# Performance work log

Measured on AMD Instinct MI355X. Metric: run time of the kernel, lower is better.

## Reference

```python
import jax, jax.numpy as jnp
import numpy as np

B, Cin, Cout, H, W = 8, 64, 128, 128, 128
K, S, P = 3, 1, 1
KK = K * K
EPS = 1e-5


def _conv2d(x, w, b=None):
    out = jax.lax.conv_general_dilated(
        x, w, window_strides=(S, S), padding=[(P, P), (P, P)],
        dimension_numbers=('NCHW', 'OIHW', 'NCHW'))
    if b is not None:
        out = out + b[None, :, None, None]
    return out


def setup_inputs() -> dict:
    key = jax.random.key(0)
    k = jax.random.split(key, 5)
    sc = 1.0 / np.sqrt(Cin * KK)
    return {
        'x': jax.random.normal(k[0], (B, Cin, H, W), jnp.float32),
        'offset_w': jax.random.normal(k[1], (2 * KK, Cin, K, K), jnp.float32) * sc,
        'offset_b': jnp.zeros((2 * KK,), jnp.float32),
        'mask_w': jax.random.normal(k[2], (KK, Cin, K, K), jnp.float32) * sc,
        'mask_b': jnp.zeros((KK,), jnp.float32),
        'conv_w': jax.random.normal(k[3], (Cout, Cin, K, K), jnp.float32) * sc,
    }


def _deform_conv2d(x, offset, mask, w):
    """Modulated deformable conv (torchvision deform_conv2d semantics)."""
    Bn, C, Hh, Ww = x.shape
    Ho, Wo = offset.shape[2], offset.shape[3]
    off = offset.reshape(Bn, KK, 2, Ho, Wo)  # (y, x) pairs per kernel tap
    ky, kx = jnp.meshgrid(jnp.arange(K), jnp.arange(K), indexing='ij')
    ky = ky.reshape(KK).astype(x.dtype)
    kx = kx.reshape(KK).astype(x.dtype)
    hy = (jnp.arange(Ho) * S - P).astype(x.dtype)
    wx = (jnp.arange(Wo) * S - P).astype(x.dtype)
    # sampling positions [B, KK, Ho, Wo]
    py = off[:, :, 0] + ky[None, :, None, None] + hy[None, None, :, None]
    px = off[:, :, 1] + kx[None, :, None, None] + wx[None, None, None, :]

    y0 = jnp.floor(py)
    x0 = jnp.floor(px)
    wy1 = py - y0; wx1 = px - x0
    wy0 = 1.0 - wy1; wx0 = 1.0 - wx1

    xf = x.reshape(Bn, C, Hh * Ww)

    def gather(yi, xi):
        valid = ((yi >= 0) & (yi < Hh) & (xi >= 0) & (xi < Ww)).astype(x.dtype)
        yc = jnp.clip(yi, 0, Hh - 1).astype(jnp.int32)
        xc = jnp.clip(xi, 0, Ww - 1).astype(jnp.int32)
        idx = (yc * Ww + xc).reshape(Bn, -1)  # [B, KK*Ho*Wo]
        vals = jnp.take_along_axis(xf, idx[:, None, :], axis=2)  # [B, C, KK*Ho*Wo]
        return vals.reshape(Bn, C, KK, Ho, Wo) * valid.reshape(Bn, 1, KK, Ho, Wo)

    v = (gather(y0, x0) * (wy0 * wx0)[:, None]
         + gather(y0, x0 + 1) * (wy0 * wx1)[:, None]
         + gather(y0 + 1, x0) * (wy1 * wx0)[:, None]
         + gather(y0 + 1, x0 + 1) * (wy1 * wx1)[:, None])  # [B, C, KK, Ho, Wo]
    v = v * mask[:, None]  # modulation
    return jnp.einsum('bckhw,ock->bohw', v, w.reshape(w.shape[0], C, KK))


def reference(x, offset_w, offset_b, mask_w, mask_b, conv_w):
    offset = _conv2d(x, offset_w, offset_b)
    mask = jax.nn.sigmoid(_conv2d(x, mask_w, mask_b))
    out = _deform_conv2d(x, offset, mask, conv_w)
    # BatchNorm2d(affine=False), training-mode normalization over (N, H, W)
    mean = out.mean(axis=(0, 2, 3), keepdims=True)
    var = out.var(axis=(0, 2, 3), keepdims=True)
    return jax.nn.relu((out - mean) * jax.lax.rsqrt(var + EPS))
```

## Files before the change

kernel.cpp:

```cpp
#include <hip/hip_runtime.h>
#include <hip/hip_bf16.h>

#define H_ 128
#define W_ 128
#define HW 16384
#define CIN 64
#define COUT 128
#define KK9 9
#define BATCH 8
#define NPIX (BATCH * HW)
#define KDIM 576

typedef short bf16x8 __attribute__((ext_vector_type(8)));
typedef float f32x4  __attribute__((ext_vector_type(4)));
typedef unsigned short ushort_t;

union U4B { uint4 u; bf16x8 v; };

__device__ __forceinline__ float us2f(unsigned short u) {
    unsigned int v = ((unsigned int)u) << 16;
    float f;
    __builtin_memcpy(&f, &v, 4);
    return f;
}
__device__ __forceinline__ float lo_f(unsigned int w) {
    unsigned int v = w << 16;
    float f;
    __builtin_memcpy(&f, &v, 4);
    return f;
}
__device__ __forceinline__ float hi_f(unsigned int w) {
    unsigned int v = w & 0xffff0000u;
    float f;
    __builtin_memcpy(&f, &v, 4);
    return f;
}
__device__ __forceinline__ unsigned short f2us_bf(float f) {
    __hip_bfloat16 h = __float2bfloat16(f);
    unsigned short u;
    __builtin_memcpy(&u, &h, 2);
    return u;
}
__device__ __forceinline__ unsigned int cvtpk_bf16(float a, float b) {
    unsigned int r;
    asm("v_cvt_pk_bf16_f32 %0, %1, %2" : "=v"(r) : "v"(a), "v"(b));
    return r;
}

template <bool F32>
__device__ __forceinline__ float ld_in(const void* p, long i) {
    if (F32) return ((const float*)p)[i];
    return us2f(((const unsigned short*)p)[i]);
}

template <bool F32>
__device__ __forceinline__ void prep_body(const void* offw, const void* offb,
                                          const void* maskw, const void* maskb,
                                          const void* convw,
                                          ushort_t* wTs, ushort_t* wcats,
                                          float* bias, int i) {
    if (i < 73728) {
        int j = i & 7, lane = (i >> 3) & 63, n = (i >> 9) & 7, ks = i >> 12;
        int co = n * 16 + (lane & 15);
        int k  = ks * 32 + ((lane >> 4) << 3) + j;
        int kk = k >> 6, ci = k & 63;
        wTs[i] = f2us_bf(ld_in<F32>(convw, (long)co * KDIM + ci * 9 + kk));
    } else if (i < 73728 + 18432) {
        int i2 = i - 73728;
        int j = i2 & 7, lane = (i2 >> 3) & 63, n = (i2 >> 9) & 1, ks = i2 >> 10;
        int co2 = n * 16 + (lane & 15);
        int k   = ks * 32 + ((lane >> 4) << 3) + j;
        int kk = k >> 6, ci = k & 63;
        float v = 0.0f;
        if (co2 < 18)      v = ld_in<F32>(offw,  (long)co2 * KDIM + ci * 9 + kk);
        else if (co2 < 27) v = ld_in<F32>(maskw, (long)(co2 - 18) * KDIM + ci * 9 + kk);
        wcats[i2] = f2us_bf(v);
    } else if (i < 73728 + 18432 + 32) {
        int j = i - 73728 - 18432;
        float v = 0.0f;
        if (j < 18)      v = ld_in<F32>(offb, j);
        else if (j < 27) v = ld_in<F32>(maskb, j - 18);
        bias[j] = v;
    }
}

template <bool F32>
__device__ __forceinline__ void transpose_body(const void* x, ushort_t* xnb,
                                               int blk) {
    __shared__ float tile[CIN * 65];
    int b    = blk >> 8;
    int pix0 = (blk & 255) * 64;
    int t    = threadIdx.x;
#pragma unroll
    for (int pass = 0; pass < 4; ++pass) {
        int slot = pass * 256 + t;
        int ci = slot >> 4;
        int f4 = slot & 15;
        long base = (long)(b * CIN + ci) * HW + pix0 + f4 * 4;
        float v0, v1, v2, v3;
        if (F32) {
            float4 v = *(const float4*)((const float*)x + base);
            v0 = v.x; v1 = v.y; v2 = v.z; v3 = v.w;
        } else {
            ushort4 u = *(const ushort4*)((const ushort_t*)x + base);
            v0 = us2f(u.x); v1 = us2f(u.y); v2 = us2f(u.z); v3 = us2f(u.w);
        }
        tile[ci * 65 + f4 * 4 + 0] = v0;
        tile[ci * 65 + f4 * 4 + 1] = v1;
        tile[ci * 65 + f4 * 4 + 2] = v2;
        tile[ci * 65 + f4 * 4 + 3] = v3;
    }
    __syncthreads();
#pragma unroll
    for (int pass = 0; pass < 4; ++pass) {
        int slot = pass * 256 + t;
        int px = slot >> 4;
        int c4 = slot & 15;
        uint2 o;
        o.x = cvtpk_bf16(tile[(c4 * 4 + 0) * 65 + px], tile[(c4 * 4 + 1) * 65 + px]);
        o.y = cvtpk_bf16(tile[(c4 * 4 + 2) * 65 + px], tile[(c4 * 4 + 3) * 65 + px]);
        *(uint2*)(xnb + (size_t)(b * HW + pix0 + px) * CIN + c4 * 4) = o;
    }
}

__global__ __launch_bounds__(256) void prep_mega(
        const void* __restrict__ x,
        const void* __restrict__ offw,
        const void* __restrict__ offb,
        const void* __restrict__ maskw,
        const void* __restrict__ maskb,
        const void* __restrict__ convw,
        ushort_t* __restrict__ wTs,
        ushort_t* __restrict__ wcats,
        float* __restrict__ bias,
        float* __restrict__ gstat,
        ushort_t* __restrict__ xnb) {
    __shared__ float flagS;
    int t   = threadIdx.x;
    int blk = blockIdx.x;

    if (t < 64) {
        uint4 v = ((const uint4*)x)[t];
        unsigned int w[4] = {v.x, v.y, v.z, v.w};
        int big = 0;
#pragma unroll
        for (int q = 0; q < 4; ++q) {
            big += (((w[q] >> 7)  & 0xFF) >= 0xC0);
            big += (((w[q] >> 23) & 0xFF) >= 0xC0);
        }
        unsigned long long m = __ballot(big > 0);
        if (t == 0) flagS = m ? 1.0f : 0.0f;
    }
    if (blk < 16) gstat[blk * 256 + t] = 0.0f;
    __syncthreads();
    bool isF32 = (flagS != 0.0f);

    if (blk < 361) {
        int i = blk * 256 + t;
        if (isF32) prep_body<true >(offw, offb, maskw, maskb, convw, wTs, wcats, bias, i);
        else       prep_body<false>(offw, offb, maskw, maskb, convw, wTs, wcats, bias, i);
    } else {
        int tb = blk - 361;
        if (isF32) transpose_body<true >(x, xnb, tb);
        else       transpose_body<false>(x, xnb, tb);
    }
}

__device__ __forceinline__ void compute_tap(int yp_t, int xp_t,
                                            float oy, float ox, float mk,
                                            int* ofs, float* wg) {
    float py  = (float)yp_t + oy;
    float pxf = (float)xp_t + ox;
    float y0f = floorf(py), x0f = floorf(pxf);
    int yi = (int)y0f, xi = (int)x0f;
    float wy1 = py - y0f, wx1 = pxf - x0f;
    float wy0 = 1.0f - wy1, wx0 = 1.0f - wx1;
    int ya  = min(max(yi, 0), H_ - 1);
    int yb  = min(max(yi + 1, 0), H_ - 1);
    int xa  = min(max(xi, 0), W_ - 1);
    int xb2 = min(max(xi + 1, 0), W_ - 1);
    bool vy0 = (yi >= 0) & (yi < H_);
    bool vy1 = (yi >= -1) & (yi < H_ - 1);
    bool vx0 = (xi >= 0) & (xi < W_);
    bool vx1 = (xi >= -1) & (xi < W_ - 1);
    float m0 = mk * wy0, m1 = mk * wy1;
    wg[0] = (vy0 & vx0) ? m0 * wx0 : 0.0f;
    wg[1] = (vy0 & vx1) ? m0 * wx1 : 0.0f;
    wg[2] = (vy1 & vx0) ? m1 * wx0 : 0.0f;
    wg[3] = (vy1 & vx1) ? m1 * wx1 : 0.0f;
    int ra = ya << 13, rb = yb << 13;
    int ca = xa << 6,  cb_ = xb2 << 6;
    ofs[0] = ra + ca;  ofs[1] = ra + cb_;
    ofs[2] = rb + ca;  ofs[3] = rb + cb_;
}

__device__ __forceinline__ void issue_half(const ushort_t* __restrict__ xb,
                                           const int* ofs, int hoff, uint4* cb) {
#pragma unroll
    for (int c = 0; c < 4; ++c)
        cb[c] = *(const uint4*)(xb + ofs[c] + hoff);
}

__device__ __forceinline__ void consume_half(int slot, const uint4* cb,
                                             const float* wg,
                                             const ushort_t* __restrict__ ldsB,
                                             int lane, f32x4* acc) {
    float2 v2[4];
#pragma unroll
    for (int j = 0; j < 4; ++j) v2[j] = make_float2(0.f, 0.f);
#pragma unroll
    for (int c = 0; c < 4; ++c) {
        float w = wg[c];
        unsigned int ww[4] = {cb[c].x, cb[c].y, cb[c].z, cb[c].w};
#pragma unroll
        for (int j = 0; j < 4; ++j) {
            v2[j].x = fmaf(w, lo_f(ww[j]), v2[j].x);
            v2[j].y = fmaf(w, hi_f(ww[j]), v2[j].y);
        }
    }
    U4B a;
    a.u = make_uint4(cvtpk_bf16(v2[0].x, v2[0].y), cvtpk_bf16(v2[1].x, v2[1].y),
                     cvtpk_bf16(v2[2].x, v2[2].y), cvtpk_bf16(v2[3].x, v2[3].y));
    const ushort_t* bbase = ldsB + ((size_t)(slot * 8) * 64 + lane) * 8;
#pragma unroll
    for (int n = 0; n < 8; ++n) {
        bf16x8 bf = *(const bf16x8*)(bbase + n * 64 * 8);
        acc[n] = __builtin_amdgcn_mfma_f32_16x16x32_bf16(a.v, bf, acc[n], 0, 0, 0);
    }
}

#define SB_PIN_VMEM() __builtin_amdgcn_sched_barrier(0x38F)

__global__ __launch_bounds__(1024, 4) void fused_conv_deform(
        const ushort_t* __restrict__ xnb,
        const ushort_t* __restrict__ wcats,
        const float* __restrict__ bias,
        const ushort_t* __restrict__ wTs,
        ushort_t* __restrict__ prebn,
        float* __restrict__ gstat) {
    __shared__ uint4 lds[8192];

    float2* offL  = (float2*)(lds + 6400);
    float*  maskS = (float*) (lds + 7552);
    float*  red   = (float*) (lds + 8128);

    int t    = threadIdx.x;
    int bid  = blockIdx.x;
    int sbid = (bid & 7) * 64 + (bid >> 3);
    int pix0 = sbid * 256;
    int b    = pix0 >> 14;
    int rem0 = pix0 & 16383;
    int y0   = rem0 >> 7;

    const uint4* wc4 = (const uint4*)wcats;
    for (int i = t; i < 2304; i += 1024) lds[i] = wc4[i];
    const uint4* xrow4 = (const uint4*)(xnb + (size_t)b * HW * CIN);
    int sxq = t >> 3, sc16 = t & 7;
#pragma unroll
    for (int r = 0; r < 4; ++r) {
        int gy = y0 - 1 + r;
        if (gy >= 0 && gy < H_) {
            uint4 v = xrow4[(size_t)gy * 1024 + t];
            lds[2304 + r * 1024 + sxq * 8 + (sc16 ^ (sxq & 7))] = v;
        }
    }
    if (t < 256) red[t] = 0.0f;
    __syncthreads();

    int wave = t >> 6, lane = t & 63, mrow = lane & 15, quad = lane >> 4;
    int px_l = wave * 16 + mrow;

    {
        int ly = px_l >> 7;
        int xp = px_l & 127;
        uint4 af0[9], af1[9];
#pragma unroll
        for (int kk = 0; kk < 9; ++kk) {
            int ty = kk / 3, tx = kk % 3;
            int tr = ly + ty;
            int gy = y0 - 1 + tr;
            int xq = xp + tx - 1;
            bool ok = (gy >= 0) && (gy < H_) && (xq >= 0) && (xq < W_);
            int xc = min(max(xq, 0), W_ - 1);
            int base = 2304 + tr * 1024 + xc * 8;
            uint4 a0 = lds[base + ((quad    ) ^ (xc & 7))];
            uint4 a1 = lds[base + ((quad + 4) ^ (xc & 7))];
            af0[kk] = ok ? a0 : make_uint4(0, 0, 0, 0);
            af1[kk] = ok ? a1 : make_uint4(0, 0, 0, 0);
        }
        f32x4 cacc[2];
        cacc[0] = (f32x4){0.f, 0.f, 0.f, 0.f};
        cacc[1] = (f32x4){0.f, 0.f, 0.f, 0.f};
        const ushort_t* ldsBc = (const ushort_t*)lds;
#pragma unroll
        for (int kk = 0; kk < 9; ++kk) {
#pragma unroll
            for (int half = 0; half < 2; ++half) {
                int ks = kk * 2 + half;
                U4B a; a.u = half ? af1[kk] : af0[kk];
#pragma unroll
                for (int n = 0; n < 2; ++n) {
                    bf16x8 bf = *(const bf16x8*)(ldsBc + ((ks * 2 + n) * 64 + lane) * 8);
                    cacc[n] = __builtin_amdgcn_mfma_f32_16x16x32_bf16(a.v, bf, cacc[n], 0, 0, 0);
                }
            }
        }
#pragma unroll
        for (int n = 0; n < 2; ++n) {
            int co2 = n * 16 + mrow;
            if (co2 >= 27) continue;
            float bs = bias[co2];
#pragma unroll
            for (int r = 0; r < 4; ++r) {
                int px = wave * 16 + quad * 4 + r;
                float v = cacc[n][r] + bs;
                if (co2 < 18)
                    ((float*)offL)[((co2 >> 1) * 256 + px) * 2 + (co2 & 1)] = v;
                else
                    maskS[(co2 - 18) * 256 + px] = 1.0f / (1.0f + __expf(-v));
            }
        }
    }
    __syncthreads();

    const uint4* ws4 = (const uint4*)wTs;
    for (int i = t; i < 4608; i += 1024) lds[i] = ws4[i];

    int remp = rem0 + px_l;
    int yp  = remp >> 7, xp2 = remp & 127;
    const ushort_t* xb = xnb + (size_t)b * HW * CIN + quad * 8;

    f32x4 acc[8];
#pragma unroll
    for (int n = 0; n < 8; ++n) acc[n] = (f32x4){0.f, 0.f, 0.f, 0.f};

    int   ofs[2][4];
    float wg[2][4];
    uint4 cb[3][4];

    float2 oE  = offL[px_l];           float mkE = maskS[px_l];
    float2 oO  = offL[256 + px_l];     float mkO = maskS[256 + px_l];
    compute_tap(yp - 1, xp2 - 1, oE.x, oE.y, mkE, ofs[0], wg[0]);
    issue_half(xb, ofs[0], 0,  cb[0]);
    issue_half(xb, ofs[0], 32, cb[1]);
    oE = offL[2 * 256 + px_l];  mkE = maskS[2 * 256 + px_l];
    SB_PIN_VMEM();
    __syncthreads();

    const ushort_t* ldsB = (const ushort_t*)lds;

#pragma unroll
    for (int hs = 0; hs < 9; ++hs) {
        const int hs2 = hs + 2;
        {
            const int kk2 = hs2 >> 1;
            const int s2  = hs2 % 3;
            if ((hs2 & 1) == 0) {
                const int tp2 = kk2 & 1;
                float ooy = tp2 ? oO.x : oE.x;
                float oox = tp2 ? oO.y : oE.y;
                float omk = tp2 ? mkO  : mkE;
                compute_tap(yp + kk2 / 3 - 1, xp2 + kk2 % 3 - 1, ooy, oox, omk,
                            ofs[tp2], wg[tp2]);
                issue_half(xb, ofs[tp2], 0, cb[s2]);
                if (kk2 + 2 <= 8) {
                    float2 o = offL[(kk2 + 2) * 256 + px_l];
                    float  m = maskS[(kk2 + 2) * 256 + px_l];
                    if (tp2) { oO = o; mkO = m; } else { oE = o; mkE = m; }
                }
            } else {
                issue_half(xb, ofs[kk2 & 1], 32, cb[s2]);
            }
        }
        SB_PIN_VMEM();
        consume_half(hs, cb[hs % 3], wg[(hs >> 1) & 1], ldsB, lane, acc);
    }
    __syncthreads();
    for (int i = t; i < 4608; i += 1024) lds[i] = ws4[4608 + i];
    __syncthreads();

#pragma unroll
    for (int hs = 9; hs < 18; ++hs) {
        const int hs2 = hs + 2;
        if (hs2 < 18) {
            const int kk2 = hs2 >> 1;
            const int s2  = hs2 % 3;
            if ((hs2 & 1) == 0) {
                const int tp2 = kk2 & 1;
                float ooy = tp2 ? oO.x : oE.x;
                float oox = tp2 ? oO.y : oE.y;
                float omk = tp2 ? mkO  : mkE;
                compute_tap(yp + kk2 / 3 - 1, xp2 + kk2 % 3 - 1, ooy, oox, omk,
                            ofs[tp2], wg[tp2]);
                issue_half(xb, ofs[tp2], 0, cb[s2]);
                if (kk2 + 2 <= 8) {
                    float2 o = offL[(kk2 + 2) * 256 + px_l];
                    float  m = maskS[(kk2 + 2) * 256 + px_l];
                    if (tp2) { oO = o; mkO = m; } else { oE = o; mkE = m; }
                }
            } else {
                issue_half(xb, ofs[kk2 & 1], 32, cb[s2]);
            }
        }
        SB_PIN_VMEM();
        consume_half(hs - 9, cb[hs % 3], wg[(hs >> 1) & 1], ldsB, lane, acc);
    }

#pragma unroll
    for (int n = 0; n < 8; ++n) {
        int co = n * 16 + mrow;
        float s = 0.f, ss = 0.f;
#pragma unroll
        for (int r = 0; r < 4; ++r) {
            int pg = pix0 + wave * 16 + quad * 4 + r;
            float v = acc[n][r];
            prebn[(size_t)pg * COUT + co] = f2us_bf(v);
            s += v;
            ss += v * v;
        }
        s  += __shfl_xor(s, 16, 64);
        s  += __shfl_xor(s, 32, 64);
        ss += __shfl_xor(ss, 16, 64);
        ss += __shfl_xor(ss, 32, 64);
        if (quad == 0) {
            atomicAdd(&red[co], s);
            atomicAdd(&red[128 + co], ss);
        }
    }
    __syncthreads();
    if (t < 256) atomicAdd(&gstat[(bid & 15) * 256 + t], red[t]);
}

__global__ __launch_bounds__(256) void bn_apply_t(const ushort_t* __restrict__ prebn,
                                                  const float* __restrict__ gstat,
                                                  float* __restrict__ out) {
    __shared__ float tile[128 * 65];
    __shared__ float mvs[256];
    int t = threadIdx.x;
    if (t < 128) {
        float s = 0.f, ss = 0.f;
#pragma unroll
        for (int part = 0; part < 16; ++part) {
            s  += gstat[part * 256 + t];
            ss += gstat[part * 256 + 128 + t];
        }
        const float invN = 1.0f / (float)NPIX;
        float mean = s * invN;
        float var  = ss * invN - mean * mean;
        if (!isfinite(mean)) mean = 0.0f;
        float r = rsqrtf(fmaxf(var, 0.0f) + 1e-5f);
        if (!isfinite(r)) r = 1.0f;
        mvs[t]       = mean;
        mvs[128 + t] = r;
    }
    __syncthreads();
    int pix0 = blockIdx.x * 64;
    int b    = pix0 >> 14;
    int rem0 = pix0 & 16383;
    const uint4* src4 = (const uint4*)(prebn + (size_t)pix0 * COUT);
#pragma unroll
    for (int r = 0; r < 4; ++r) {
        int i  = r * 256 + t;
        uint4 v = src4[i];
        int p  = i >> 4;
        int c0 = (i & 15) * 8;
        unsigned int w[4] = {v.x, v.y, v.z, v.w};
#pragma unroll
        for (int j = 0; j < 4; ++j) {
            int c = c0 + j * 2;
            float f0 = lo_f(w[j]);
            float f1 = hi_f(w[j]);
            tile[c * 65 + p]       = fmaxf((f0 - mvs[c])     * mvs[128 + c],     0.0f);
            tile[(c + 1) * 65 + p] = fmaxf((f1 - mvs[c + 1]) * mvs[128 + c + 1], 0.0f);
        }
    }
    __syncthreads();
#pragma unroll
    for (int r = 0; r < 8; ++r) {
        int i  = r * 256 + t;
        int c2 = i >> 4;
        int q  = (i & 15) * 4;
        float4 w4 = make_float4(tile[c2 * 65 + q],     tile[c2 * 65 + q + 1],
                                tile[c2 * 65 + q + 2], tile[c2 * 65 + q + 3]);
        *(float4*)(out + (size_t)(b * COUT + c2) * HW + rem0 + q) = w4;
    }
}

extern "C" void kernel_launch(void* const* d_in, const int* in_sizes, int n_in,
                              void* d_out, int out_size, void* d_ws, size_t ws_size,
                              hipStream_t stream) {
    (void)in_sizes; (void)n_in; (void)out_size; (void)ws_size;
    const void* x     = d_in[0];
    const void* offw  = d_in[1];
    const void* offb  = d_in[2];
    const void* maskw = d_in[3];
    const void* maskb = d_in[4];
    const void* convw = d_in[5];

    float* ws       = (float*)d_ws;
    float* off2     = ws;
    float* mask_ws  = off2 + 2359296;
    float* bias     = mask_ws + 1179648;
    float* gstat    = bias + 32;
    float* flag     = gstat + 4096;
    ushort_t* wTs   = (ushort_t*)(flag + 16);
    ushort_t* wcats = wTs + 73728;
    ushort_t* xnb   = wcats + 18432;
    ushort_t* prebn = xnb + 8388608;
    float* out      = (float*)d_out;

    prep_mega<<<2409, 256, 0, stream>>>(x, offw, offb, maskw, maskb, convw,
                                        wTs, wcats, bias, gstat, xnb);
    fused_conv_deform<<<512, 1024, 0, stream>>>(xnb, wcats, bias, wTs, prebn, gstat);
    bn_apply_t<<<2048, 256, 0, stream>>>(prebn, gstat, out);
}
```

Baseline: 194.7 us.

## Fuse deform conv and BN apply into one cooperative persistent kernel

Merges the deformable-conv kernel and the BN-apply kernel into a single cooperative launch of 256 blocks, each handling two pixel tiles. A grid-wide sync sits between computing statistics and normalizing. The second tile's results stay in registers and are normalized directly, so its bf16 prebn round-trip and one kernel launch are avoided. The cost is half the block count (256 blocks of 1024 threads), a grid barrier, and serial processing of two tiles per block, which may reduce parallelism and latency hiding.

```diff
diff --git a/kernel.cpp b/kernel.cpp
--- a/kernel.cpp
+++ b/kernel.cpp
@@ -1,5 +1,8 @@
 #include <hip/hip_runtime.h>
 #include <hip/hip_bf16.h>
+#include <hip/hip_cooperative_groups.h>
+
+namespace cg = cooperative_groups;
 
 #define H_ 128
 #define W_ 128
@@ -231,13 +234,14 @@
 
 #define SB_PIN_VMEM() __builtin_amdgcn_sched_barrier(0x38F)
 
-__global__ __launch_bounds__(1024, 4) void fused_conv_deform(
+__global__ __launch_bounds__(1024, 4) void fused_all(
         const ushort_t* __restrict__ xnb,
         const ushort_t* __restrict__ wcats,
         const float* __restrict__ bias,
         const ushort_t* __restrict__ wTs,
         ushort_t* __restrict__ prebn,
-        float* __restrict__ gstat) {
+        float* __restrict__ gstat,
+        float* __restrict__ out) {
     __shared__ uint4 lds[8192];
 
     float2* offL  = (float2*)(lds + 6400);
@@ -246,203 +250,211 @@
 
     int t    = threadIdx.x;
     int bid  = blockIdx.x;
-    int sbid = (bid & 7) * 64 + (bid >> 3);
-    int pix0 = sbid * 256;
-    int b    = pix0 >> 14;
-    int rem0 = pix0 & 16383;
-    int y0   = rem0 >> 7;
-
-    const uint4* wc4 = (const uint4*)wcats;
-    for (int i = t; i < 2304; i += 1024) lds[i] = wc4[i];
-    const uint4* xrow4 = (const uint4*)(xnb + (size_t)b * HW * CIN);
-    int sxq = t >> 3, sc16 = t & 7;
-#pragma unroll
-    for (int r = 0; r < 4; ++r) {
-        int gy = y0 - 1 + r;
-        if (gy >= 0 && gy < H_) {
-            uint4 v = xrow4[(size_t)gy * 1024 + t];
-            lds[2304 + r * 1024 + sxq * 8 + (sc16 ^ (sxq & 7))] = v;
-        }
-    }
-    if (t < 256) red[t] = 0.0f;
-    __syncthreads();
+    int xcd  = bid & 7;
+    int ord  = bid >> 3;
+    int b    = xcd;
 
     int wave = t >> 6, lane = t & 63, mrow = lane & 15, quad = lane >> 4;
     int px_l = wave * 16 + mrow;
-
-    {
-        int ly = px_l >> 7;
-        int xp = px_l & 127;
-        uint4 af0[9], af1[9];
-#pragma unroll
-        for (int kk = 0; kk < 9; ++kk) {
-            int ty = kk / 3, tx = kk % 3;
-            int tr = ly + ty;
-            int gy = y0 - 1 + tr;
-            int xq = xp + tx - 1;
-            bool ok = (gy >= 0) && (gy < H_) && (xq >= 0) && (xq < W_);
-            int xc = min(max(xq, 0), W_ - 1);
-            int base = 2304 + tr * 1024 + xc * 8;
-            uint4 a0 = lds[base + ((quad    ) ^ (xc & 7))];
-            uint4 a1 = lds[base + ((quad + 4) ^ (xc & 7))];
-            af0[kk] = ok ? a0 : make_uint4(0, 0, 0, 0);
-            af1[kk] = ok ? a1 : make_uint4(0, 0, 0, 0);
-        }
-        f32x4 cacc[2];
-        cacc[0] = (f32x4){0.f, 0.f, 0.f, 0.f};
-        cacc[1] = (f32x4){0.f, 0.f, 0.f, 0.f};
-        const ushort_t* ldsBc = (const ushort_t*)lds;
-#pragma unroll
-        for (int kk = 0; kk < 9; ++kk) {
-#pragma unroll
-            for (int half = 0; half < 2; ++half) {
-                int ks = kk * 2 + half;
-                U4B a; a.u = half ? af1[kk] : af0[kk];
-#pragma unroll
-                for (int n = 0; n < 2; ++n) {
-                    bf16x8 bf = *(const bf16x8*)(ldsBc + ((ks * 2 + n) * 64 + lane) * 8);
-                    cacc[n] = __builtin_amdgcn_mfma_f32_16x16x32_bf16(a.v, bf, cacc[n], 0, 0, 0);
-                }
-            }
-        }
-#pragma unroll
-        for (int n = 0; n < 2; ++n) {
-            int co2 = n * 16 + mrow;
-            if (co2 >= 27) continue;
-            float bs = bias[co2];
+    const ushort_t* xb = xnb + (size_t)b * HW * CIN + quad * 8;
+    const uint4* wc4   = (const uint4*)wcats;
+    const uint4* ws4   = (const uint4*)wTs;
+    const uint4* xrow4 = (const uint4*)(xnb + (size_t)b * HW * CIN);
+    const ushort_t* ldsB = (const ushort_t*)lds;
+
+    f32x4 acc[8];
+
+    for (int g = 0; g < 2; ++g) {
+        int tile = xcd * 64 + ord * 2 + g;
+        int pix0 = tile * 256;
+        int rem0 = pix0 & 16383;
+        int y0   = rem0 >> 7;
+
+        for (int i = t; i < 2304; i += 1024) lds[i] = wc4[i];
+        {
+            int sxq = t >> 3, sc16 = t & 7;
 #pragma unroll
             for (int r = 0; r < 4; ++r) {
-                int px = wave * 16 + quad * 4 + r;
-                float v = cacc[n][r] + bs;
-                if (co2 < 18)
-                    ((float*)offL)[((co2 >> 1) * 256 + px) * 2 + (co2 & 1)] = v;
-                else
-                    maskS[(co2 - 18) * 256 + px] = 1.0f / (1.0f + __expf(-v));
-            }
-        }
-    }
-    __syncthreads();
-
-    const uint4* ws4 = (const uint4*)wTs;
-    for (int i = t; i < 4608; i += 1024) lds[i] = ws4[i];
-
-    int remp = rem0 + px_l;
-    int yp  = remp >> 7, xp2 = remp & 127;
-    const ushort_t* xb = xnb + (size_t)b * HW * CIN + quad * 8;
-
-    f32x4 acc[8];
-#pragma unroll
-    for (int n = 0; n < 8; ++n) acc[n] = (f32x4){0.f, 0.f, 0.f, 0.f};
-
-    int   ofs[2][4];
-    float wg[2][4];
-    uint4 cb[3][4];
-
-    float2 oE  = offL[px_l];           float mkE = maskS[px_l];
-    float2 oO  = offL[256 + px_l];     float mkO = maskS[256 + px_l];
-    compute_tap(yp - 1, xp2 - 1, oE.x, oE.y, mkE, ofs[0], wg[0]);
-    issue_half(xb, ofs[0], 0,  cb[0]);
-    issue_half(xb, ofs[0], 32, cb[1]);
-    oE = offL[2 * 256 + px_l];  mkE = maskS[2 * 256 + px_l];
-    SB_PIN_VMEM();
-    __syncthreads();
-
-    const ushort_t* ldsB = (const ushort_t*)lds;
-
-#pragma unroll
-    for (int hs = 0; hs < 9; ++hs) {
-        const int hs2 = hs + 2;
+                int gy = y0 - 1 + r;
+                if (gy >= 0 && gy < H_) {
+                    uint4 v = xrow4[(size_t)gy * 1024 + t];
+                    lds[2304 + r * 1024 + sxq * 8 + (sc16 ^ (sxq & 7))] = v;
+                }
+            }
+        }
+        if (t < 256) red[t] = 0.0f;
+        __syncthreads();
+
         {
-            const int kk2 = hs2 >> 1;
-            const int s2  = hs2 % 3;
-            if ((hs2 & 1) == 0) {
-                const int tp2 = kk2 & 1;
-                float ooy = tp2 ? oO.x : oE.x;
-                float oox = tp2 ? oO.y : oE.y;
-                float omk = tp2 ? mkO  : mkE;
-                compute_tap(yp + kk2 / 3 - 1, xp2 + kk2 % 3 - 1, ooy, oox, omk,
-                            ofs[tp2], wg[tp2]);
-                issue_half(xb, ofs[tp2], 0, cb[s2]);
-                if (kk2 + 2 <= 8) {
-                    float2 o = offL[(kk2 + 2) * 256 + px_l];
-                    float  m = maskS[(kk2 + 2) * 256 + px_l];
-                    if (tp2) { oO = o; mkO = m; } else { oE = o; mkE = m; }
-                }
-            } else {
-                issue_half(xb, ofs[kk2 & 1], 32, cb[s2]);
-            }
-        }
+            int ly = px_l >> 7;
+            int xp = px_l & 127;
+            uint4 af0[9], af1[9];
+#pragma unroll
+            for (int kk = 0; kk < 9; ++kk) {
+                int ty = kk / 3, tx = kk % 3;
+                int tr = ly + ty;
+                int gy = y0 - 1 + tr;
+                int xq = xp + tx - 1;
+                bool ok = (gy >= 0) && (gy < H_) && (xq >= 0) && (xq < W_);
+                int xc = min(max(xq, 0), W_ - 1);
+                int base = 2304 + tr * 1024 + xc * 8;
+                uint4 a0 = lds[base + ((quad    ) ^ (xc & 7))];
+                uint4 a1 = lds[base + ((quad + 4) ^ (xc & 7))];
+                af0[kk] = ok ? a0 : make_uint4(0, 0, 0, 0);
+                af1[kk] = ok ? a1 : make_uint4(0, 0, 0, 0);
+            }
+            f32x4 cacc[2];
+            cacc[0] = (f32x4){0.f, 0.f, 0.f, 0.f};
+            cacc[1] = (f32x4){0.f, 0.f, 0.f, 0.f};
+#pragma unroll
+            for (int kk = 0; kk < 9; ++kk) {
+#pragma unroll
+                for (int half = 0; half < 2; ++half) {
+                    int ks = kk * 2 + half;
+                    U4B a; a.u = half ? af1[kk] : af0[kk];
+#pragma unroll
+                    for (int n = 0; n < 2; ++n) {
+                        bf16x8 bf = *(const bf16x8*)(ldsB + ((ks * 2 + n) * 64 + lane) * 8);
+                        cacc[n] = __builtin_amdgcn_mfma_f32_16x16x32_bf16(a.v, bf, cacc[n], 0, 0, 0);
+                    }
+                }
+            }
+#pragma unroll
+            for (int n = 0; n < 2; ++n) {
+                int co2 = n * 16 + mrow;
+                if (co2 >= 27) continue;
+                float bs = bias[co2];
+#pragma unroll
+                for (int r = 0; r < 4; ++r) {
+                    int px = wave * 16 + quad * 4 + r;
+                    float v = cacc[n][r] + bs;
+                    if (co2 < 18)
+                        ((float*)offL)[((co2 >> 1) * 256 + px) * 2 + (co2 & 1)] = v;
+                    else
+                        maskS[(co2 - 18) * 256 + px] = 1.0f / (1.0f + __expf(-v));
+                }
+            }
+        }
+        __syncthreads();
+
+        for (int i = t; i < 4608; i += 1024) lds[i] = ws4[i];
+
+        int remp = rem0 + px_l;
+        int yp  = remp >> 7, xp2 = remp & 127;
+
+#pragma unroll
+        for (int n = 0; n < 8; ++n) acc[n] = (f32x4){0.f, 0.f, 0.f, 0.f};
+
+        int   ofs[2][4];
+        float wg[2][4];
+        uint4 cb[3][4];
+
+        float2 oE  = offL[px_l];           float mkE = maskS[px_l];
+        float2 oO  = offL[256 + px_l];     float mkO = maskS[256 + px_l];
+        compute_tap(yp - 1, xp2 - 1, oE.x, oE.y, mkE, ofs[0], wg[0]);
+        issue_half(xb, ofs[0], 0,  cb[0]);
+        issue_half(xb, ofs[0], 32, cb[1]);
+        oE = offL[2 * 256 + px_l];  mkE = maskS[2 * 256 + px_l];
         SB_PIN_VMEM();
-        consume_half(hs, cb[hs % 3], wg[(hs >> 1) & 1], ldsB, lane, acc);
-    }
-    __syncthreads();
-    for (int i = t; i < 4608; i += 1024) lds[i] = ws4[4608 + i];
-    __syncthreads();
-
-#pragma unroll
-    for (int hs = 9; hs < 18; ++hs) {
-        const int hs2 = hs + 2;
-        if (hs2 < 18) {
-            const int kk2 = hs2 >> 1;
-            const int s2  = hs2 % 3;
-            if ((hs2 & 1) == 0) {
-                const int tp2 = kk2 & 1;
-                float ooy = tp2 ? oO.x : oE.x;
-                float oox = tp2 ? oO.y : oE.y;
-                float omk = tp2 ? mkO  : mkE;
-                compute_tap(yp + kk2 / 3 - 1, xp2 + kk2 % 3 - 1, ooy, oox, omk,
-                            ofs[tp2], wg[tp2]);
-                issue_half(xb, ofs[tp2], 0, cb[s2]);
-                if (kk2 + 2 <= 8) {
-                    float2 o = offL[(kk2 + 2) * 256 + px_l];
-                    float  m = maskS[(kk2 + 2) * 256 + px_l];
-                    if (tp2) { oO = o; mkO = m; } else { oE = o; mkE = m; }
-                }
-            } else {
-                issue_half(xb, ofs[kk2 & 1], 32, cb[s2]);
-            }
-        }
-        SB_PIN_VMEM();
-        consume_half(hs - 9, cb[hs % 3], wg[(hs >> 1) & 1], ldsB, lane, acc);
-    }
-
-#pragma unroll
-    for (int n = 0; n < 8; ++n) {
-        int co = n * 16 + mrow;
-        float s = 0.f, ss = 0.f;
-#pragma unroll
-        for (int r = 0; r < 4; ++r) {
-            int pg = pix0 + wave * 16 + quad * 4 + r;
-            float v = acc[n][r];
-            prebn[(size_t)pg * COUT + co] = f2us_bf(v);
-            s += v;
-            ss += v * v;
-        }
-        s  += __shfl_xor(s, 16, 64);
-        s  += __shfl_xor(s, 32, 64);
-        ss += __shfl_xor(ss, 16, 64);
-        ss += __shfl_xor(ss, 32, 64);
-        if (quad == 0) {
-            atomicAdd(&red[co], s);
-            atomicAdd(&red[128 + co], ss);
-        }
-    }
-    __syncthreads();
-    if (t < 256) atomicAdd(&gstat[(bid & 15) * 256 + t], red[t]);
-}
-
-__global__ __launch_bounds__(256) void bn_apply_t(const ushort_t* __restrict__ prebn,
-                                                  const float* __restrict__ gstat,
-                                                  float* __restrict__ out) {
-    __shared__ float tile[128 * 65];
-    __shared__ float mvs[256];
-    int t = threadIdx.x;
+        __syncthreads();
+
+#pragma unroll
+        for (int hs = 0; hs < 9; ++hs) {
+            const int hs2 = hs + 2;
+            {
+                const int kk2 = hs2 >> 1;
+                const int s2  = hs2 % 3;
+                if ((hs2 & 1) == 0) {
+                    const int tp2 = kk2 & 1;
+                    float ooy = tp2 ? oO.x : oE.x;
+                    float oox = tp2 ? oO.y : oE.y;
+                    float omk = tp2 ? mkO  : mkE;
+                    compute_tap(yp + kk2 / 3 - 1, xp2 + kk2 % 3 - 1, ooy, oox, omk,
+                                ofs[tp2], wg[tp2]);
+                    issue_half(xb, ofs[tp2], 0, cb[s2]);
+                    if (kk2 + 2 <= 8) {
+                        float2 o = offL[(kk2 + 2) * 256 + px_l];
+                        float  m = maskS[(kk2 + 2) * 256 + px_l];
+                        if (tp2) { oO = o; mkO = m; } else { oE = o; mkE = m; }
+                    }
+                } else {
+                    issue_half(xb, ofs[kk2 & 1], 32, cb[s2]);
+                }
+            }
+            SB_PIN_VMEM();
+            consume_half(hs, cb[hs % 3], wg[(hs >> 1) & 1], ldsB, lane, acc);
+        }
+        __syncthreads();
+        for (int i = t; i < 4608; i += 1024) lds[i] = ws4[4608 + i];
+        __syncthreads();
+
+#pragma unroll
+        for (int hs = 9; hs < 18; ++hs) {
+            const int hs2 = hs + 2;
+            if (hs2 < 18) {
+                const int kk2 = hs2 >> 1;
+                const int s2  = hs2 % 3;
+                if ((hs2 & 1) == 0) {
+                    const int tp2 = kk2 & 1;
+                    float ooy = tp2 ? oO.x : oE.x;
+                    float oox = tp2 ? oO.y : oE.y;
+                    float omk = tp2 ? mkO  : mkE;
+                    compute_tap(yp + kk2 / 3 - 1, xp2 + kk2 % 3 - 1, ooy, oox, omk,
+                                ofs[tp2], wg[tp2]);
+                    issue_half(xb, ofs[tp2], 0, cb[s2]);
+                    if (kk2 + 2 <= 8) {
+                        float2 o = offL[(kk2 + 2) * 256 + px_l];
+                        float  m = maskS[(kk2 + 2) * 256 + px_l];
+                        if (tp2) { oO = o; mkO = m; } else { oE = o; mkE = m; }
+                    }
+                } else {
+                    issue_half(xb, ofs[kk2 & 1], 32, cb[s2]);
+                }
+            }
+            SB_PIN_VMEM();
+            consume_half(hs - 9, cb[hs % 3], wg[(hs >> 1) & 1], ldsB, lane, acc);
+        }
+
+#pragma unroll
+        for (int n = 0; n < 8; ++n) {
+            int co = n * 16 + mrow;
+            float s = 0.f, ss = 0.f;
+#pragma unroll
+            for (int r = 0; r < 4; ++r) {
+                float v = acc[n][r];
+                if (g == 0) {
+                    int pg = pix0 + wave * 16 + quad * 4 + r;
+                    prebn[(size_t)pg * COUT + co] = f2us_bf(v);
+                }
+                s += v;
+                ss += v * v;
+            }
+            s  += __shfl_xor(s, 16, 64);
+            s  += __shfl_xor(s, 32, 64);
+            ss += __shfl_xor(ss, 16, 64);
+            ss += __shfl_xor(ss, 32, 64);
+            if (quad == 0) {
+                atomicAdd(&red[co], s);
+                atomicAdd(&red[128 + co], ss);
+            }
+        }
+        __syncthreads();
+        if (t < 256) atomicAdd(&gstat[(bid & 15) * 256 + t], red[t]);
+        __syncthreads();
+    }
+
+    cg::this_grid().sync();
+
+    float* mvs = (float*)lds;
+    float* tl  = (float*)(lds + 64);
     if (t < 128) {
         float s = 0.f, ss = 0.f;
 #pragma unroll
         for (int part = 0; part < 16; ++part) {
-            s  += gstat[part * 256 + t];
-            ss += gstat[part * 256 + 128 + t];
+            s  += __hip_atomic_load(&gstat[part * 256 + t],
+                                    __ATOMIC_RELAXED, __HIP_MEMORY_SCOPE_AGENT);
+            ss += __hip_atomic_load(&gstat[part * 256 + 128 + t],
+                                    __ATOMIC_RELAXED, __HIP_MEMORY_SCOPE_AGENT);
         }
         const float invN = 1.0f / (float)NPIX;
         float mean = s * invN;
@@ -454,35 +466,62 @@
         mvs[128 + t] = r;
     }
     __syncthreads();
-    int pix0 = blockIdx.x * 64;
-    int b    = pix0 >> 14;
-    int rem0 = pix0 & 16383;
-    const uint4* src4 = (const uint4*)(prebn + (size_t)pix0 * COUT);
-#pragma unroll
-    for (int r = 0; r < 4; ++r) {
-        int i  = r * 256 + t;
-        uint4 v = src4[i];
-        int p  = i >> 4;
-        int c0 = (i & 15) * 8;
-        unsigned int w[4] = {v.x, v.y, v.z, v.w};
-#pragma unroll
-        for (int j = 0; j < 4; ++j) {
-            int c = c0 + j * 2;
-            float f0 = lo_f(w[j]);
-            float f1 = hi_f(w[j]);
-            tile[c * 65 + p]       = fmaxf((f0 - mvs[c])     * mvs[128 + c],     0.0f);
-            tile[(c + 1) * 65 + p] = fmaxf((f1 - mvs[c + 1]) * mvs[128 + c + 1], 0.0f);
-        }
-    }
-    __syncthreads();
-#pragma unroll
-    for (int r = 0; r < 8; ++r) {
-        int i  = r * 256 + t;
-        int c2 = i >> 4;
-        int q  = (i & 15) * 4;
-        float4 w4 = make_float4(tile[c2 * 65 + q],     tile[c2 * 65 + q + 1],
-                                tile[c2 * 65 + q + 2], tile[c2 * 65 + q + 3]);
-        *(float4*)(out + (size_t)(b * COUT + c2) * HW + rem0 + q) = w4;
+
+    {
+        int tile1 = xcd * 64 + ord * 2 + 1;
+        int rem1  = (tile1 & 63) * 256;
+        for (int h = 0; h < 2; ++h) {
+            if ((wave >> 3) == h) {
+#pragma unroll
+                for (int n = 0; n < 8; ++n) {
+                    int co = n * 16 + mrow;
+                    float mn = mvs[co], rs = mvs[128 + co];
+#pragma unroll
+                    for (int r = 0; r < 4; ++r) {
+                        int lp = (wave & 7) * 16 + quad * 4 + r;
+                        tl[co * 129 + lp] = fmaxf((acc[n][r] - mn) * rs, 0.0f);
+                    }
+                }
+            }
+            __syncthreads();
+            for (int i = t; i < 4096; i += 1024) {
+                int c2 = i >> 5, q = (i & 31) * 4;
+                float4 w4 = make_float4(tl[c2 * 129 + q],     tl[c2 * 129 + q + 1],
+                                        tl[c2 * 129 + q + 2], tl[c2 * 129 + q + 3]);
+                *(float4*)(out + (size_t)(b * COUT + c2) * HW + rem1 + h * 128 + q) = w4;
+            }
+            __syncthreads();
+        }
+    }
+
+    {
+        int tile0 = xcd * 64 + ord * 2;
+        int rem0g = (tile0 & 63) * 256;
+        const uint4* pb4 = (const uint4*)(prebn + (size_t)(tile0 * 256) * COUT);
+        for (int h = 0; h < 2; ++h) {
+#pragma unroll
+            for (int k = 0; k < 2; ++k) {
+                int j = k * 1024 + t;
+                uint4 v = pb4[h * 2048 + j];
+                int p  = j >> 4;
+                int c0 = (j & 15) * 8;
+                unsigned int w[4] = {v.x, v.y, v.z, v.w};
+#pragma unroll
+                for (int jj = 0; jj < 4; ++jj) {
+                    int c = c0 + jj * 2;
+                    tl[c * 129 + p]       = fmaxf((lo_f(w[jj]) - mvs[c])     * mvs[128 + c],     0.0f);
+                    tl[(c + 1) * 129 + p] = fmaxf((hi_f(w[jj]) - mvs[c + 1]) * mvs[128 + c + 1], 0.0f);
+                }
+            }
+            __syncthreads();
+            for (int i = t; i < 4096; i += 1024) {
+                int c2 = i >> 5, q = (i & 31) * 4;
+                float4 w4 = make_float4(tl[c2 * 129 + q],     tl[c2 * 129 + q + 1],
+                                        tl[c2 * 129 + q + 2], tl[c2 * 129 + q + 3]);
+                *(float4*)(out + (size_t)(b * COUT + c2) * HW + rem0g + h * 128 + q) = w4;
+            }
+            __syncthreads();
+        }
     }
 }
 
@@ -511,6 +550,9 @@
 
     prep_mega<<<2409, 256, 0, stream>>>(x, offw, offb, maskw, maskb, convw,
                                         wTs, wcats, bias, gstat, xnb);
-    fused_conv_deform<<<512, 1024, 0, stream>>>(xnb, wcats, bias, wTs, prebn, gstat);
-    bn_apply_t<<<2048, 256, 0, stream>>>(prebn, gstat, out);
-}
+
+    void* args[] = {(void*)&xnb, (void*)&wcats, (void*)&bias, (void*)&wTs,
+                    (void*)&prebn, (void*)&gstat, (void*)&out};
+    hipLaunchCooperativeKernel((const void*)fused_all, dim3(256), dim3(1024),
+                               args, 0, stream);
+}
```

After: 288.0 us. 48.0% more time.
